# Kernel optimization log

Hardware: AMD Instinct MI355X
Metric: run time of the kernel (lower is better)

Reference implementation:

```python
import jax, jax.numpy as jnp
import numpy as np
import math

D_MODEL = 1024
N_HEADS = 16
D_K = D_MODEL // N_HEADS
B, S = 4, 1024
MAX_REL = 64  # table built for 2*64-1 positions, clamped beyond


def setup_inputs() -> dict:
    key = jax.random.key(0)
    ks = jax.random.split(key, 11)
    init = 1.0 / math.sqrt(D_MODEL)
    def lin(k):
        kw, kb = jax.random.split(k)
        W = jax.random.uniform(kw, (D_MODEL, D_MODEL), jnp.float32, -init, init)
        b = jax.random.uniform(kb, (D_MODEL,), jnp.float32, -init, init)
        return W, b
    wq, bq = lin(ks[0]); wk, bk = lin(ks[1]); wv, bv = lin(ks[2]); wo, bo = lin(ks[3])
    x = jax.random.normal(ks[4], (B, S, D_MODEL), jnp.float32)
    rel_table = jax.random.normal(ks[5], (2 * MAX_REL - 1, N_HEADS), jnp.float32)
    mask = jnp.ones((B, 1, 1, S), jnp.int32)
    return {"x": x, "mask": mask, "wq": wq, "bq": bq, "wk": wk, "bk": bk,
            "wv": wv, "bv": bv, "wo": wo, "bo": bo, "rel_table": rel_table}


def reference(x, mask, wq, bq, wk, bk, wv, bv, wo, bo, rel_table):
    Bn, Sn, Dm = x.shape
    scale = math.sqrt(D_K)
    def heads(y):  # [B,S,D] -> [B,H,S,dk]
        return y.reshape(Bn, Sn, N_HEADS, D_K).transpose(0, 2, 1, 3)
    Q = heads(x @ wq.T + bq)
    K = heads(x @ wk.T + bk)
    V = heads(x @ wv.T + bv)
    scores = jnp.einsum('bhqd,bhkd->bhqk', Q, K) / scale
    # relative position bias gather, clamped to table range
    rel = jnp.arange(Sn)[None, :] - jnp.arange(Sn)[:, None] + MAX_REL - 1
    rel = jnp.clip(rel, 0, 2 * MAX_REL - 2)
    bias = rel_table[rel]                      # [S,S,H]
    scores = scores + bias.transpose(2, 0, 1)[None]  # [B,H,S,S]
    scores = jnp.where(mask == 0, jnp.float32(-1e9), scores)
    attn = jax.nn.softmax(scores, axis=-1)
    ctx = jnp.einsum('bhqk,bhkd->bhqd', attn, V)
    ctx = ctx.transpose(0, 2, 1, 3).reshape(Bn, Sn, Dm)
    return ctx @ wo.T + bo
```

## Files before the change

### kernel.cpp

```cpp
#include <hip/hip_runtime.h>
#include <hip/hip_bf16.h>

typedef __attribute__((ext_vector_type(8))) short short8;
typedef __attribute__((ext_vector_type(4))) short short4v;
typedef __attribute__((ext_vector_type(4))) float f32x4;

#define D_MODEL 1024
#define N_HEADS 16
#define D_KK 64
#define BATCH 4
#define SEQ 1024
#define NTOK (BATCH*SEQ)

#define LOG2E  1.44269504f
#define SCALE2 (0.125f * 1.44269504f)
#define NEGBIG (-1.44269504e9f)

#if __has_builtin(__builtin_amdgcn_mfma_f32_16x16x16bf16_1k)
#define HAVE_MFMA16 1
#else
#define HAVE_MFMA16 0
#endif

#if __has_builtin(__builtin_amdgcn_exp2f)
#define EXP2(x) __builtin_amdgcn_exp2f(x)
#else
#define EXP2(x) exp2f(x)
#endif

template<int N> struct ic { static constexpr int value = N; };

__device__ __forceinline__ short f2b(float f){
  unsigned u = __float_as_uint(f);
  u += 0x7fffu + ((u >> 16) & 1u);
  return (short)(u >> 16);
}

__device__ __forceinline__ void gl2lds16(const void* g, void* l){
  __builtin_amdgcn_global_load_lds(
      (const __attribute__((address_space(1))) void*)g,
      (__attribute__((address_space(3))) void*)l, 16, 0, 0);
}

__device__ __forceinline__ float max3f(float a, float b, float c){
  float d; asm("v_max3_f32 %0, %1, %2, %3" : "=v"(d) : "v"(a), "v"(b), "v"(c)); return d;
}
__device__ __forceinline__ float tmax16(const f32x4* sc){
  float t = max3f(sc[0][0], sc[0][1], sc[0][2]);
  t = max3f(t, sc[0][3], sc[1][0]);
  t = max3f(t, sc[1][1], sc[1][2]);
  t = max3f(t, sc[1][3], sc[2][0]);
  t = max3f(t, sc[2][1], sc[2][2]);
  t = max3f(t, sc[2][3], sc[3][0]);
  t = max3f(t, sc[3][1], sc[3][2]);
  return fmaxf(t, sc[3][3]);
}

__global__ __launch_bounds__(256) void cvt_all_kernel(
    const float* __restrict__ x,  const float* __restrict__ wq,
    const float* __restrict__ wk, const float* __restrict__ wv,
    const float* __restrict__ wo, short* __restrict__ dst)
{
  const size_t NX = (size_t)NTOK * D_MODEL;
  const size_t NW = (size_t)D_MODEL * D_MODEL;
  size_t e = ((size_t)blockIdx.x * 256 + threadIdx.x) * 4;
  const float* s;
  size_t off;
  if      (e < NX)        { s = x;  off = e; }
  else if (e < NX +   NW) { s = wq; off = e - NX; }
  else if (e < NX + 2*NW) { s = wk; off = e - NX -   NW; }
  else if (e < NX + 3*NW) { s = wv; off = e - NX - 2*NW; }
  else                    { s = wo; off = e - NX - 3*NW; }
  f32x4 v = *reinterpret_cast<const f32x4*>(s + off);
  short4v o;
  o[0]=f2b(v[0]); o[1]=f2b(v[1]); o[2]=f2b(v[2]); o[3]=f2b(v[3]);
  *reinterpret_cast<short4v*>(dst + e) = o;
}

template<int BN, int MODE, bool PRESC>
__device__ __forceinline__ void gemm_bt_body(const short* __restrict__ A,
    const short* __restrict__ W, const float* __restrict__ bias,
    void* __restrict__ Cout, int N, int K, int bm0, int bn0,
    short* AsB, short* BsB)
{
  constexpr int NF = BN / 32;
  const int tid = threadIdx.x, lane = tid & 63, w = tid >> 6;
  const int wr = w >> 1, wc = w & 1;
  const int srow = lane >> 3;
  const int scol = ((lane & 7) ^ srow) * 8;
  const int fr = lane & 15, g = lane >> 4;

  f32x4 acc[4][NF];
  #pragma unroll
  for (int m=0;m<4;m++)
    #pragma unroll
    for (int n=0;n<NF;n++) acc[m][n] = (f32x4){0.f,0.f,0.f,0.f};

  for (int k0 = 0; k0 < K; k0 += 64){
    __syncthreads();
    #pragma unroll
    for (int i=0;i<4;i++){
      const int c = w*4 + i;
      gl2lds16(A + (size_t)(bm0 + c*8 + srow)*K + k0 + scol, &AsB[c*8*64]);
    }
    #pragma unroll
    for (int i=0;i<NF;i++){
      const int c = w*NF + i;
      gl2lds16(W + (size_t)(bn0 + c*8 + srow)*K + k0 + scol, &BsB[c*8*64]);
    }
    __syncthreads();
    #pragma unroll
    for (int f=0; f<2; f++){
      short8 af[4], bfr[NF];
      #pragma unroll
      for (int m=0;m<4;m++){
        const int rr = wr*64 + m*16 + fr;
        af[m] = *reinterpret_cast<const short8*>(
            (const char*)AsB + rr*128 + ((g*16 + f*64) ^ ((rr&7)<<4)));
      }
      #pragma unroll
      for (int n=0;n<NF;n++){
        const int rr = wc*(BN/2) + n*16 + fr;
        bfr[n] = *reinterpret_cast<const short8*>(
            (const char*)BsB + rr*128 + ((g*16 + f*64) ^ ((rr&7)<<4)));
      }
      #pragma unroll
      for (int m=0;m<4;m++)
        #pragma unroll
        for (int n=0;n<NF;n++)
          acc[m][n] = __builtin_amdgcn_mfma_f32_16x16x32_bf16(af[m], bfr[n], acc[m][n], 0,0,0);
    }
  }

  #pragma unroll
  for (int n=0;n<NF;n++){
    const int col = bn0 + wc*(BN/2) + n*16 + fr;
    const float bv = bias[col];
    if (MODE == 2){
      const int hh = col >> 6, dd = col & 63;
      #pragma unroll
      for (int m=0;m<4;m++){
        const int row0 = bm0 + wr*64 + m*16 + g*4;
        const int bb = row0 >> 10, ss = row0 & 1023;
        short4v o;
        #pragma unroll
        for (int r=0;r<4;r++){
          float v = acc[m][n][r] + bv;
          if (PRESC) v *= SCALE2;
          o[r] = f2b(v);
        }
        *reinterpret_cast<short4v*>(
            (short*)Cout + ((size_t)(bb*N_HEADS+hh)*D_KK + dd)*SEQ + ss) = o;
      }
    } else {
      #pragma unroll
      for (int m=0;m<4;m++){
        const int row0 = bm0 + wr*64 + m*16 + g*4;
        #pragma unroll
        for (int r=0;r<4;r++){
          float v = acc[m][n][r] + bv;
          if (PRESC) v *= SCALE2;
          if (MODE == 1) ((float*)Cout)[(size_t)(row0+r)*N + col] = v;
          else           ((short*)Cout)[(size_t)(row0+r)*N + col] = f2b(v);
        }
      }
    }
  }
}

__global__ __launch_bounds__(256) void qkv_gemm_kernel(
    const short* __restrict__ X,
    const short* __restrict__ Wq, const short* __restrict__ Wk, const short* __restrict__ Wv,
    const float* __restrict__ bq, const float* __restrict__ bk, const float* __restrict__ bv,
    short* __restrict__ Q, short* __restrict__ K, short* __restrict__ V)
{
  __shared__ short As[128*64];
  __shared__ short Bs[64*64];
  const int bid = blockIdx.x;
  const int xcd = bid & 7, s = bid >> 3;
  const int z = s >> 6;
  const int rem = s & 63;
  const int bn0 = (rem >> 2) * 64;
  const int bm0 = (xcd * 4 + (rem & 3)) * 128;
  if (z == 0)      gemm_bt_body<64,0,true >(X, Wq, bq, Q, D_MODEL, D_MODEL, bm0, bn0, As, Bs);
  else if (z == 1) gemm_bt_body<64,0,false>(X, Wk, bk, K, D_MODEL, D_MODEL, bm0, bn0, As, Bs);
  else             gemm_bt_body<64,2,false>(X, Wv, bv, V, D_MODEL, D_MODEL, bm0, bn0, As, Bs);
}

__global__ __launch_bounds__(256) void out_gemm_kernel(
    const short* __restrict__ Ctx, const short* __restrict__ Wo,
    const float* __restrict__ bo, float* __restrict__ Out)
{
  __shared__ short As[128*64];
  __shared__ short Bs[64*64];
  const int bid = blockIdx.x;
  const int xcd = bid & 7, s = bid >> 3;
  const int bn0 = (s >> 2) * 64;
  const int bm0 = (xcd * 4 + (s & 3)) * 128;
  gemm_bt_body<64,1,false>(Ctx, Wo, bo, Out, D_MODEL, D_MODEL, bm0, bn0, As, Bs);
}

__global__ __launch_bounds__(512, 2) void attn_kernel(
    const short* __restrict__ Qb, const short* __restrict__ Kb,
    const short* __restrict__ Vtg, const int* __restrict__ mask,
    const float* __restrict__ rel_table, short* __restrict__ Ctx)
{
  const int bid = blockIdx.x;
  const int xcd = bid & 7, slot = bid >> 3;
  const int bh = xcd * 8 + (slot >> 3);
  const int qt = slot & 7;
  const int b = bh >> 4, h = bh & 15;
  const int q0 = qt * 128;
  const int tid = threadIdx.x, lane = tid & 63, w = tid >> 6;
  const int team = w >> 2, wt = w & 3;
  const int fr = lane & 15, g = lane >> 4;

  __shared__ short kvbuf[2][2][2][64][64];
  __shared__ float rel_pad[384];
  __shared__ float mbias[2][2][64];
  __shared__ float ml[128][2];

  for (int i = tid; i < 384; i += 512){
    int d = i - 128;
    d = d < 0 ? 0 : (d > 126 ? 126 : d);
    rel_pad[i] = rel_table[d * N_HEADS + h] * LOG2E;
  }
  const float cb_lo = rel_table[0*N_HEADS + h]   * LOG2E;
  const float cb_hi = rel_table[126*N_HEADS + h] * LOG2E;

  const short* Qg = Qb + (size_t)b*SEQ*D_MODEL + h*D_KK;
  const short* Kg = Kb + (size_t)b*SEQ*D_MODEL + h*D_KK;
  const short* Vg = Vtg + (size_t)bh*D_KK*SEQ;

  const int qa = q0 + wt*32 + fr;
  const int qb = qa + 16;
  short8 qfa[2], qfb[2];
  #pragma unroll
  for (int f=0; f<2; f++){
    qfa[f] = *reinterpret_cast<const short8*>(Qg + (size_t)qa*D_MODEL + g*8 + f*32);
    qfb[f] = *reinterpret_cast<const short8*>(Qg + (size_t)qb*D_MODEL + g*8 + f*32);
  }

  const char* lds0 = (const char*)kvbuf;
  const int swzb = (fr & 7) << 4;
  const char* kp[2];
  #pragma unroll
  for (int f=0; f<2; f++)
    kp[f] = lds0 + team*16384 + fr*128 + ((g*16 + f*64) ^ swzb);
  const char* vp[4];
  #pragma unroll
  for (int kt=0; kt<4; kt++)
    vp[kt] = lds0 + 32768 + team*16384 + fr*128
           + ((((kt*2 + (g>>1)) ^ (fr&7)) << 4) + (g&1)*8);
  const char* mbp = (const char*)mbias + team*512 + g*16;

  f32x4 ctxa[4], ctxb[4];
  #pragma unroll
  for (int dt=0; dt<4; dt++){ ctxa[dt] = (f32x4){0.f,0.f,0.f,0.f}; ctxb[dt] = ctxa[dt]; }
  float mruna = -3.0e38f, lruna = 0.f, mrunb = -3.0e38f, lrunb = 0.f;

  const int srow = lane >> 3;
  const int scol = ((lane & 7) ^ srow) * 8;
  auto stage = [&](int buf, int kv0){
    #pragma unroll
    for (int i=0;i<2;i++){
      const int c = wt*2 + i;
      gl2lds16(Kg + (size_t)(kv0 + c*8 + srow)*D_MODEL + scol, &kvbuf[0][team][buf][c*8][0]);
      gl2lds16(Vg + (size_t)(c*8 + srow)*SEQ + kv0 + scol,     &kvbuf[1][team][buf][c*8][0]);
    }
    if (wt == 0){
      const int delta = kv0 - q0;
      const bool far = (delta <= -128 || delta >= 192);
      const float cb = far ? (delta > 0 ? cb_hi : cb_lo) : 0.f;
      mbias[team][buf][lane] = mask[b*SEQ + kv0 + lane] ? cb : NEGBIG;
    }
  };

  auto tile_step = [&](auto BUFC, int kv0) __attribute__((always_inline)) {
    constexpr int BUFL = decltype(BUFC)::value;

    f32x4 sca[4], scb[4];
    const int delta = kv0 - q0;
    if (delta <= -128 || delta >= 192){
      #pragma unroll
      for (int kt=0;kt<4;kt++){
        f32x4 mb4 = *reinterpret_cast<const f32x4*>(mbp + (BUFL*256 + kt*64));
        sca[kt] = mb4;
        scb[kt] = mb4;
      }
    } else {
      const int pbase = delta + 63 - (wt*32 + fr) + 128 + g*4;
      f32x4 rr[5];
      #pragma unroll
      for (int j=0;j<5;j++)
        #pragma unroll
        for (int r=0;r<4;r++)
          rr[j][r] = rel_pad[pbase - 16 + j*16 + r];
      #pragma unroll
      for (int kt=0;kt<4;kt++){
        f32x4 mb4 = *reinterpret_cast<const f32x4*>(mbp + (BUFL*256 + kt*64));
        #pragma unroll
        for (int r=0;r<4;r++){
          sca[kt][r] = rr[kt+1][r] + mb4[r];
          scb[kt][r] = rr[kt][r]   + mb4[r];
        }
      }
    }

    __builtin_amdgcn_s_setprio(1);
    #pragma unroll
    for (int kt=0;kt<4;kt++){
      #pragma unroll
      for (int f=0;f<2;f++){
        short8 kf = *reinterpret_cast<const short8*>(kp[f] + (kt*2048 + BUFL*8192));
        sca[kt] = __builtin_amdgcn_mfma_f32_16x16x32_bf16(kf, qfa[f], sca[kt], 0,0,0);
        scb[kt] = __builtin_amdgcn_mfma_f32_16x16x32_bf16(kf, qfb[f], scb[kt], 0,0,0);
      }
    }
    __builtin_amdgcn_s_setprio(0);

    short4v paa[4], pab[4];
    {
      const float tmax = tmax16(sca);
      if (!__all(tmax <= mruna + 8.f)){
        float tm = fmaxf(tmax, __shfl_xor(tmax, 16));
        tm = fmaxf(tm, __shfl_xor(tm, 32));
        const float mnew = fmaxf(mruna, tm);
        const float corr = EXP2(mruna - mnew);
        lruna *= corr;
        #pragma unroll
        for (int dt=0;dt<4;dt++)
          #pragma unroll
          for (int r=0;r<4;r++) ctxa[dt][r] *= corr;
        mruna = mnew;
      }
      float psum = 0.f;
      #pragma unroll
      for (int kt=0;kt<4;kt++){
        float p0 = EXP2(sca[kt][0] - mruna);
        float p1 = EXP2(sca[kt][1] - mruna);
        float p2 = EXP2(sca[kt][2] - mruna);
        float p3 = EXP2(sca[kt][3] - mruna);
        psum += (p0 + p1) + (p2 + p3);
        union { short4v s; __hip_bfloat162 hh[2]; } u;
        u.hh[0] = __float22bfloat162_rn(make_float2(p0, p1));
        u.hh[1] = __float22bfloat162_rn(make_float2(p2, p3));
        paa[kt] = u.s;
      }
      lruna += psum;
    }
    {
      const float tmax = tmax16(scb);
      if (!__all(tmax <= mrunb + 8.f)){
        float tm = fmaxf(tmax, __shfl_xor(tmax, 16));
        tm = fmaxf(tm, __shfl_xor(tm, 32));
        const float mnew = fmaxf(mrunb, tm);
        const float corr = EXP2(mrunb - mnew);
        lrunb *= corr;
        #pragma unroll
        for (int dt=0;dt<4;dt++)
          #pragma unroll
          for (int r=0;r<4;r++) ctxb[dt][r] *= corr;
        mrunb = mnew;
      }
      float psum = 0.f;
      #pragma unroll
      for (int kt=0;kt<4;kt++){
        float p0 = EXP2(scb[kt][0] - mrunb);
        float p1 = EXP2(scb[kt][1] - mrunb);
        float p2 = EXP2(scb[kt][2] - mrunb);
        float p3 = EXP2(scb[kt][3] - mrunb);
        psum += (p0 + p1) + (p2 + p3);
        union { short4v s; __hip_bfloat162 hh[2]; } u;
        u.hh[0] = __float22bfloat162_rn(make_float2(p0, p1));
        u.hh[1] = __float22bfloat162_rn(make_float2(p2, p3));
        pab[kt] = u.s;
      }
      lrunb += psum;
    }

    __builtin_amdgcn_s_setprio(1);
#if HAVE_MFMA16
    #pragma unroll
    for (int dt=0;dt<4;dt++){
      #pragma unroll
      for (int kt=0;kt<4;kt++){
        short4v va = *reinterpret_cast<const short4v*>(vp[kt] + (dt*2048 + BUFL*8192));
        ctxa[dt] = __builtin_amdgcn_mfma_f32_16x16x16bf16_1k(va, paa[kt], ctxa[dt], 0,0,0);
        ctxb[dt] = __builtin_amdgcn_mfma_f32_16x16x16bf16_1k(va, pab[kt], ctxb[dt], 0,0,0);
      }
    }
#else
    const char* vsb = lds0 + 32768 + team*16384 + BUFL*8192;
    #pragma unroll
    for (int f=0;f<2;f++){
      union { short8 s8; unsigned u[4]; } bfa, bfb;
      #pragma unroll
      for (int m=0;m<4;m++){
        const int srcl = ((g&1)*2 + (m>>1))*16 + fr;
        union { short4v s; unsigned u[2]; } ca0, ca1, cb0, cb1;
        ca0.s = paa[f*2+0]; ca1.s = paa[f*2+1];
        cb0.s = pab[f*2+0]; cb1.s = pab[f*2+1];
        unsigned a0 = __shfl((int)ca0.u[m&1], srcl);
        unsigned a1 = __shfl((int)ca1.u[m&1], srcl);
        bfa.u[m] = (g >> 1) ? a1 : a0;
        unsigned b0 = __shfl((int)cb0.u[m&1], srcl);
        unsigned b1 = __shfl((int)cb1.u[m&1], srcl);
        bfb.u[m] = (g >> 1) ? b1 : b0;
      }
      #pragma unroll
      for (int dt=0;dt<4;dt++){
        const int dr = dt*16 + fr;
        const int vswz = (dr & 7) << 4;
        short8 va = *reinterpret_cast<const short8*>(
            vsb + dr*128 + ((g*16 + f*64) ^ vswz));
        ctxa[dt] = __builtin_amdgcn_mfma_f32_16x16x32_bf16(va, bfa.s8, ctxa[dt], 0,0,0);
        ctxb[dt] = __builtin_amdgcn_mfma_f32_16x16x32_bf16(va, bfb.s8, ctxb[dt], 0,0,0);
      }
    }
#endif
    __builtin_amdgcn_s_setprio(0);

    __syncthreads();
  };

  const int kvbase = team * 512;
  stage(0, kvbase);
  __syncthreads();

  for (int t = 0; t < 8; t += 2){
    const int kv0 = kvbase + t * 64;
    stage(1, kv0 + 64);
    tile_step(ic<0>{}, kv0);
    if (t < 6) stage(0, kv0 + 128);
    tile_step(ic<1>{}, kv0 + 64);
  }

  lruna += __shfl_xor(lruna, 16);
  lruna += __shfl_xor(lruna, 32);
  lrunb += __shfl_xor(lrunb, 16);
  lrunb += __shfl_xor(lrunb, 32);

  float* mctx = (float*)&kvbuf[0][0][0][0][0];
  const int rowA = wt*32 + fr, rowB = rowA + 16;
  if (team == 1){
    #pragma unroll
    for (int dt=0;dt<4;dt++){
      *reinterpret_cast<f32x4*>(&mctx[rowA*72 + dt*16 + g*4]) = ctxa[dt];
      *reinterpret_cast<f32x4*>(&mctx[rowB*72 + dt*16 + g*4]) = ctxb[dt];
    }
    ml[rowA][0] = mruna; ml[rowA][1] = lruna;
    ml[rowB][0] = mrunb; ml[rowB][1] = lrunb;
  }
  __syncthreads();
  if (team == 0){
    {
      const float m1 = ml[rowA][0], l1 = ml[rowA][1];
      const float m  = fmaxf(mruna, m1);
      const float s0 = EXP2(mruna - m), s1 = EXP2(m1 - m);
      const float rl = 1.f / (lruna*s0 + l1*s1);
      #pragma unroll
      for (int dt=0;dt<4;dt++){
        f32x4 c1 = *reinterpret_cast<const f32x4*>(&mctx[rowA*72 + dt*16 + g*4]);
        short4v o;
        #pragma unroll
        for (int r=0;r<4;r++) o[r] = f2b((ctxa[dt][r]*s0 + c1[r]*s1) * rl);
        *reinterpret_cast<short4v*>(
            Ctx + (size_t)(b*SEQ + qa)*D_MODEL + h*D_KK + dt*16 + g*4) = o;
      }
    }
    {
      const float m1 = ml[rowB][0], l1 = ml[rowB][1];
      const float m  = fmaxf(mrunb, m1);
      const float s0 = EXP2(mrunb - m), s1 = EXP2(m1 - m);
      const float rl = 1.f / (lrunb*s0 + l1*s1);
      #pragma unroll
      for (int dt=0;dt<4;dt++){
        f32x4 c1 = *reinterpret_cast<const f32x4*>(&mctx[rowB*72 + dt*16 + g*4]);
        short4v o;
        #pragma unroll
        for (int r=0;r<4;r++) o[r] = f2b((ctxb[dt][r]*s0 + c1[r]*s1) * rl);
        *reinterpret_cast<short4v*>(
            Ctx + (size_t)(b*SEQ + qb)*D_MODEL + h*D_KK + dt*16 + g*4) = o;
      }
    }
  }
}

extern "C" void kernel_launch(void* const* d_in, const int* in_sizes, int n_in,
                              void* d_out, int out_size, void* d_ws, size_t ws_size,
                              hipStream_t stream) {
  const float* x    = (const float*)d_in[0];
  const int*   mask = (const int*)  d_in[1];
  const float* wq   = (const float*)d_in[2];
  const float* bq   = (const float*)d_in[3];
  const float* wk   = (const float*)d_in[4];
  const float* bk   = (const float*)d_in[5];
  const float* wv   = (const float*)d_in[6];
  const float* bv   = (const float*)d_in[7];
  const float* wo   = (const float*)d_in[8];
  const float* bo   = (const float*)d_in[9];
  const float* rel  = (const float*)d_in[10];

  const size_t NX = (size_t)NTOK * D_MODEL;
  const size_t NW = (size_t)D_MODEL * D_MODEL;
  if (ws_size < (NX + 4*NW + 4*NX) * sizeof(short)) return;
  short* xb   = (short*)d_ws;
  short* wqb  = xb  + NX;
  short* wkb  = wqb + NW;
  short* wvb  = wkb + NW;
  short* wob  = wvb + NW;
  short* Qb   = wob + NW;
  short* Kb   = Qb  + NX;
  short* Vtg  = Kb  + NX;
  short* Ctxb = Vtg + NX;

  cvt_all_kernel<<<8192, 256, 0, stream>>>(x, wq, wk, wv, wo, xb);

  qkv_gemm_kernel<<<1536, 256, 0, stream>>>(
      xb, wqb, wkb, wvb, bq, bk, bv, Qb, Kb, Vtg);

  attn_kernel<<<512, 512, 0, stream>>>(Qb, Kb, Vtg, mask, rel, Ctxb);

  out_gemm_kernel<<<512, 256, 0, stream>>>(Ctxb, wob, bo, (float*)d_out);
}
```

Baseline: 105.2 us.

## Deepen K/V prefetch with explicit vmcnt waits and precompute mask bias

Restructures the attention tile loop so two K/V tiles are always in flight. Each step waits with a partial s_waitcnt vmcnt(4) plus a raw barrier instead of a full __syncthreads that drains all loads. The mask/bias row for all eight tiles is precomputed into LDS once at kernel start, removing the per-stage mask loads. This should hide global-to-LDS latency better, but it relies on exact vmcnt accounting of the gl2lds instructions, and any miscount could cause races.

```diff
diff --git a/kernel.cpp b/kernel.cpp
--- a/kernel.cpp
+++ b/kernel.cpp
@@ -217,7 +217,7 @@
 
   __shared__ short kvbuf[2][2][2][64][64];
   __shared__ float rel_pad[384];
-  __shared__ float mbias[2][2][64];
+  __shared__ float mb_all[2][8][64];
   __shared__ float ml[128][2];
 
   for (int i = tid; i < 384; i += 512){
@@ -227,6 +227,15 @@
   }
   const float cb_lo = rel_table[0*N_HEADS + h]   * LOG2E;
   const float cb_hi = rel_table[126*N_HEADS + h] * LOG2E;
+
+  for (int e = tid; e < 1024; e += 512){
+    const int tm = e >> 9, tt = (e >> 6) & 7, i = e & 63;
+    const int kvt = tm*512 + tt*64;
+    const int delta = kvt - q0;
+    const bool far = (delta <= -128 || delta >= 192);
+    const float cb = far ? (delta > 0 ? cb_hi : cb_lo) : 0.f;
+    mb_all[tm][tt][i] = mask[b*SEQ + kvt + i] ? cb : NEGBIG;
+  }
 
   const short* Qg = Qb + (size_t)b*SEQ*D_MODEL + h*D_KK;
   const short* Kg = Kb + (size_t)b*SEQ*D_MODEL + h*D_KK;
@@ -252,7 +261,7 @@
   for (int kt=0; kt<4; kt++)
     vp[kt] = lds0 + 32768 + team*16384 + fr*128
            + ((((kt*2 + (g>>1)) ^ (fr&7)) << 4) + (g&1)*8);
-  const char* mbp = (const char*)mbias + team*512 + g*16;
+  const char* mbp0 = (const char*)mb_all + team*2048 + g*16;
 
   f32x4 ctxa[4], ctxb[4];
   #pragma unroll
@@ -268,23 +277,25 @@
       gl2lds16(Kg + (size_t)(kv0 + c*8 + srow)*D_MODEL + scol, &kvbuf[0][team][buf][c*8][0]);
       gl2lds16(Vg + (size_t)(c*8 + srow)*SEQ + kv0 + scol,     &kvbuf[1][team][buf][c*8][0]);
     }
-    if (wt == 0){
-      const int delta = kv0 - q0;
-      const bool far = (delta <= -128 || delta >= 192);
-      const float cb = far ? (delta > 0 ? cb_hi : cb_lo) : 0.f;
-      mbias[team][buf][lane] = mask[b*SEQ + kv0 + lane] ? cb : NEGBIG;
-    }
   };
 
-  auto tile_step = [&](auto BUFC, int kv0) __attribute__((always_inline)) {
+  auto tile_step = [&](auto BUFC, auto VMC, int kv0, int tt) __attribute__((always_inline)) {
     constexpr int BUFL = decltype(BUFC)::value;
+    constexpr int VM   = decltype(VMC)::value;
+
+    if constexpr (VM == 4) asm volatile("s_waitcnt vmcnt(4)" ::: "memory");
+    else                   asm volatile("s_waitcnt vmcnt(0)" ::: "memory");
+    __builtin_amdgcn_s_barrier();
+    asm volatile("" ::: "memory");
+
+    const char* mbp = mbp0 + tt*256;
 
     f32x4 sca[4], scb[4];
     const int delta = kv0 - q0;
     if (delta <= -128 || delta >= 192){
       #pragma unroll
       for (int kt=0;kt<4;kt++){
-        f32x4 mb4 = *reinterpret_cast<const f32x4*>(mbp + (BUFL*256 + kt*64));
+        f32x4 mb4 = *reinterpret_cast<const f32x4*>(mbp + kt*64);
         sca[kt] = mb4;
         scb[kt] = mb4;
       }
@@ -298,7 +309,7 @@
           rr[j][r] = rel_pad[pbase - 16 + j*16 + r];
       #pragma unroll
       for (int kt=0;kt<4;kt++){
-        f32x4 mb4 = *reinterpret_cast<const f32x4*>(mbp + (BUFL*256 + kt*64));
+        f32x4 mb4 = *reinterpret_cast<const f32x4*>(mbp + kt*64);
         #pragma unroll
         for (int r=0;r<4;r++){
           sca[kt][r] = rr[kt+1][r] + mb4[r];
@@ -421,20 +432,24 @@
 #endif
     __builtin_amdgcn_s_setprio(0);
 
-    __syncthreads();
+    asm volatile("" ::: "memory");
+    __builtin_amdgcn_s_barrier();
   };
 
   const int kvbase = team * 512;
+  __syncthreads();
   stage(0, kvbase);
-  __syncthreads();
-
-  for (int t = 0; t < 8; t += 2){
-    const int kv0 = kvbase + t * 64;
-    stage(1, kv0 + 64);
-    tile_step(ic<0>{}, kv0);
-    if (t < 6) stage(0, kv0 + 128);
-    tile_step(ic<1>{}, kv0 + 64);
-  }
+  stage(1, kvbase + 64);
+
+  for (int t = 0; t < 6; t += 2){
+    tile_step(ic<0>{}, ic<4>{}, kvbase + t*64,     t);
+    stage(0, kvbase + (t+2)*64);
+    tile_step(ic<1>{}, ic<4>{}, kvbase + (t+1)*64, t+1);
+    stage(1, kvbase + (t+3)*64);
+  }
+  tile_step(ic<0>{}, ic<4>{}, kvbase + 6*64, 6);
+  tile_step(ic<1>{}, ic<0>{}, kvbase + 7*64, 7);
+  asm volatile("" ::: "memory");
 
   lruna += __shfl_xor(lruna, 16);
   lruna += __shfl_xor(lruna, 32);
```

Result: no change. 103.8 us (-1.4%).
